# Kernel tuning notes

Hardware: AMD Instinct MI355X
Metric: run time of the kernel (lower is better)

## Reference

```python
import jax, jax.numpy as jnp
import numpy as np

D_MODEL = 1024
NUM_HEADS = 16
D_K = D_MODEL // NUM_HEADS
B, S = 2, 2048
NEG = -1.0e9


def setup_inputs() -> dict:
    key = jax.random.key(0)
    ks = jax.random.split(key, 10)
    inp = {
        'query': jax.random.normal(ks[0], (B, S, D_MODEL), dtype=jnp.float32),
        'key':   jax.random.normal(ks[1], (B, S, D_MODEL), dtype=jnp.float32),
        'value': jax.random.normal(ks[2], (B, S, D_MODEL), dtype=jnp.float32),
        'mask':  jax.random.randint(ks[3], (B, S, S), 0, 2, dtype=jnp.int32),
        # nn.Linear params (weight [out,in], bias [out])
        'Wq': jax.random.normal(ks[4], (D_MODEL, D_MODEL), dtype=jnp.float32) * 0.02,
        'bq': jnp.zeros((D_MODEL,), dtype=jnp.float32),
        'Wk': jax.random.normal(ks[5], (D_MODEL, D_MODEL), dtype=jnp.float32) * 0.02,
        'bk': jnp.zeros((D_MODEL,), dtype=jnp.float32),
        'Wv': jax.random.normal(ks[6], (D_MODEL, D_MODEL), dtype=jnp.float32) * 0.02,
        'bv': jnp.zeros((D_MODEL,), dtype=jnp.float32),
    }
    return inp


def reference(query, key, value, mask, Wq, bq, Wk, bk, Wv, bv):
    b = query.shape[0]
    # projections: nn.Linear -> x @ W.T + b
    Q = query @ Wq.T + bq
    K = key @ Wk.T + bk
    V = value @ Wv.T + bv
    # [B, H, S, d_k]
    Q = Q.reshape(b, -1, NUM_HEADS, D_K).transpose(0, 2, 1, 3)
    K = K.reshape(b, -1, NUM_HEADS, D_K).transpose(0, 2, 1, 3)
    V = V.reshape(b, -1, NUM_HEADS, D_K).transpose(0, 2, 1, 3)
    scale = 1.0 / np.sqrt(D_K).astype(np.float32)
    scores = jnp.einsum('bhqd,bhkd->bhqk', Q, K) * scale  # [B,H,S,S]
    scores = jnp.where(mask[:, None, :, :] == 0, NEG, scores)
    attn_weights = jax.nn.softmax(scores, axis=-1)
    out = jnp.einsum('bhqk,bhkd->bhqd', attn_weights, V)
    out = out.transpose(0, 2, 1, 3).reshape(b, -1, D_MODEL)
    return out, attn_weights
```

## Files before the change

### kernel.cpp

```cpp
#include <hip/hip_runtime.h>
#include <hip/hip_bf16.h>
#include <cstdint>
#include <cstddef>

#define S_LEN 2048
#define DM 1024
#define NEGV -1.0e9f

typedef __attribute__((ext_vector_type(8))) short bf16x8;
typedef __attribute__((ext_vector_type(4))) float f32x4;
typedef __attribute__((ext_vector_type(4))) unsigned short us4;
typedef __attribute__((ext_vector_type(4))) int i32x4;
typedef __attribute__((ext_vector_type(4))) unsigned int ui32x4;
typedef __attribute__((ext_vector_type(2))) unsigned int u32x2;

__device__ __forceinline__ unsigned short f2bf(float f) {
  unsigned int u = __float_as_uint(f);
  unsigned int r = (u + 0x7fffu + ((u >> 16) & 1u)) >> 16;
  return (unsigned short)r;
}

__device__ __forceinline__ unsigned int pack_bf2(float a, float b) {
  return (unsigned int)f2bf(a) | ((unsigned int)f2bf(b) << 16);
}

__device__ __forceinline__ void async_copy16(const void* g, void* l) {
  __builtin_amdgcn_global_load_lds((const __attribute__((address_space(1))) void*)g,
                                   (__attribute__((address_space(3))) void*)l, 16, 0, 0);
}

__global__ __launch_bounds__(256) void cvt_all(
    const float* __restrict__ q, const float* __restrict__ k, const float* __restrict__ v,
    const float* __restrict__ wq, const float* __restrict__ wk, const float* __restrict__ wv,
    unsigned short* __restrict__ qb, unsigned short* __restrict__ kb2, unsigned short* __restrict__ vb,
    unsigned short* __restrict__ wqb, unsigned short* __restrict__ wkb, unsigned short* __restrict__ wvb) {
  const int gid = blockIdx.x * 256 + threadIdx.x;
  const float* src; unsigned short* dst; int idx;
  if (gid < 3145728) {
    const int j = gid >> 20; idx = gid & 1048575;
    src = (j == 0) ? q : (j == 1) ? k : v;
    dst = (j == 0) ? qb : (j == 1) ? kb2 : vb;
  } else {
    const int g = gid - 3145728;
    const int j = g >> 18; idx = g & 262143;
    src = (j == 0) ? wq : (j == 1) ? wk : wv;
    dst = (j == 0) ? wqb : (j == 1) ? wkb : wvb;
  }
  const float4 vv = reinterpret_cast<const float4*>(src)[idx];
  us4 o;
  o[0] = f2bf(vv.x); o[1] = f2bf(vv.y); o[2] = f2bf(vv.z); o[3] = f2bf(vv.w);
  reinterpret_cast<us4*>(dst)[idx] = o;
}

__global__ __launch_bounds__(256) void maskbits_kernel(const int* __restrict__ mask,
                                                       unsigned int* __restrict__ mb) {
  const int idx = blockIdx.x * 256 + threadIdx.x;
  const int row = idx >> 6, w = idx & 63;
  const int* src = mask + (size_t)row * S_LEN + w * 32;
  unsigned int r = 0;
#pragma unroll
  for (int j = 0; j < 8; ++j) {
    const i32x4 v = *(const i32x4*)(src + j * 4);
    r |= (v[0] ? 1u : 0u) << (j * 4 + 0);
    r |= (v[1] ? 1u : 0u) << (j * 4 + 1);
    r |= (v[2] ? 1u : 0u) << (j * 4 + 2);
    r |= (v[3] ? 1u : 0u) << (j * 4 + 3);
  }
  mb[(size_t)row * 64 + w] = r;
}

__global__ __launch_bounds__(256) void proj_gemm(
    const unsigned short* __restrict__ Xq, const unsigned short* __restrict__ Wqw,
    const float* __restrict__ bq, unsigned short* __restrict__ Cq,
    const unsigned short* __restrict__ Xk, const unsigned short* __restrict__ Wkw,
    const float* __restrict__ bk, unsigned short* __restrict__ Ck,
    const unsigned short* __restrict__ Xv, const unsigned short* __restrict__ Wvw,
    const float* __restrict__ bv, unsigned short* __restrict__ Cv) {
  const int bid = blockIdx.x;
  const int c = bid & 7, s = bid >> 3;
  const int n0 = (s & 7) * 128;
  const int mzg = c * 12 + (s >> 3);
  const int m0 = (mzg & 31) * 128;
  const int z = mzg >> 5;

  const unsigned short* X; const unsigned short* W; const float* bias; unsigned short* C;
  if (z == 0)      { X = Xq; W = Wqw; bias = bq; C = Cq; }
  else if (z == 1) { X = Xk; W = Wkw; bias = bk; C = Ck; }
  else             { X = Xv; W = Wvw; bias = bv; C = Cv; }

  __shared__ unsigned short Ab[128 * 64];
  __shared__ unsigned short Bb[128 * 64];

  const int t  = threadIdx.x;
  const int wv2 = t >> 6, l = t & 63;
  const int lr = l & 15, lg = l >> 4;
  const int wr = wv2 >> 1, wc = wv2 & 1;

  const f32x4 fz = {0.f, 0.f, 0.f, 0.f};
  f32x4 acc[4][4];
#pragma unroll
  for (int m = 0; m < 4; ++m)
#pragma unroll
    for (int n = 0; n < 4; ++n) acc[m][n] = fz;

  const int srow = t >> 3;
  const int sc16 = t & 7;

  for (int kt = 0; kt < 16; ++kt) {
    const int kb = kt * 64;
#pragma unroll
    for (int it = 0; it < 4; ++it) {
      const int row = it * 32 + srow;
      const int c16 = sc16 ^ (row & 7);
      const unsigned short* gA = X + (size_t)(m0 + row) * DM + kb + c16 * 8;
      const unsigned short* gB = W + (size_t)(n0 + row) * DM + kb + c16 * 8;
      async_copy16(gA, (char*)Ab + it * 4096 + wv2 * 1024);
      async_copy16(gB, (char*)Bb + it * 4096 + wv2 * 1024);
    }
    __syncthreads();
#pragma unroll
    for (int kk = 0; kk < 2; ++kk) {
      bf16x8 af[4], bfr[4];
      const int c16 = kk * 4 + lg;
      const int sw = (c16 ^ (lr & 7)) * 16;
#pragma unroll
      for (int m = 0; m < 4; ++m) {
        const int row = wr * 64 + m * 16 + lr;
        af[m] = *(const bf16x8*)((const char*)Ab + row * 128 + sw);
      }
#pragma unroll
      for (int n = 0; n < 4; ++n) {
        const int row = wc * 64 + n * 16 + lr;
        bfr[n] = *(const bf16x8*)((const char*)Bb + row * 128 + sw);
      }
#pragma unroll
      for (int m = 0; m < 4; ++m)
#pragma unroll
        for (int n = 0; n < 4; ++n)
          acc[m][n] = __builtin_amdgcn_mfma_f32_16x16x32_bf16(af[m], bfr[n], acc[m][n], 0, 0, 0);
    }
    __syncthreads();
  }

#pragma unroll
  for (int n = 0; n < 4; ++n) {
    const int ccol = n0 + wc * 64 + n * 16 + lr;
    const float bb = bias[ccol];
#pragma unroll
    for (int m = 0; m < 4; ++m) {
      const int crow0 = m0 + wr * 64 + m * 16 + lg * 4;
#pragma unroll
      for (int j = 0; j < 4; ++j)
        C[(size_t)(crow0 + j) * DM + ccol] = f2bf(acc[m][n][j] + bb);
    }
  }
}

__global__ __launch_bounds__(256) void kpack_kernel(const unsigned short* __restrict__ Kp,
                                                    unsigned short* __restrict__ Kpack) {
  const int tid = blockIdx.x * 256 + threadIdx.x;
  const int lane = tid & 63;
  const int chunk = (tid >> 6) & 1;
  const int kb = (tid >> 7) & 127;
  const int h = (tid >> 14) & 15;
  const int b = tid >> 18;
  const unsigned short* src = Kp + (size_t)(b * 2048 + kb * 16 + (lane & 15)) * 1024
                                 + h * 64 + chunk * 32 + (lane >> 4) * 8;
  unsigned short* dst = Kpack + ((size_t)((b * 16 + h) * 128 + kb) * 2 + chunk) * 512 + lane * 8;
  *(bf16x8*)dst = *(const bf16x8*)src;
}

__global__ __launch_bounds__(256) void vtranspack_kernel(const unsigned short* __restrict__ Vp,
                                                         unsigned short* __restrict__ Vpack) {
  __shared__ unsigned short tile[64][72];
  const int id = blockIdx.x;
  const int pr = id & 3;
  const int w  = (id >> 2) & 7;
  const int h  = (id >> 5) & 15;
  const int b  = id >> 9;
  const int t  = threadIdx.x;
  const int R0 = b * 2048 + w * 256 + pr * 64;
  const int C0 = h * 64;
  {
    const int row = t >> 2, q = t & 3;
    const unsigned short* src = Vp + (size_t)(R0 + row) * 1024 + C0 + q * 16;
    *(bf16x8*)&tile[row][q * 16] = *(const bf16x8*)src;
    *(bf16x8*)&tile[row][q * 16 + 8] = *(const bf16x8*)(src + 8);
  }
  __syncthreads();
  unsigned short* dstb = Vpack + ((size_t)(b * 16 + h) * 256 + (w * 4 + pr) * 8) * 512;
#pragma unroll
  for (int p2 = 0; p2 < 2; ++p2) {
    const int cid = p2 * 256 + t;
    const int blk = cid >> 6;
    const int lane = cid & 63;
    const int s2 = blk >> 2, n = blk & 3;
    unsigned short v[8];
#pragma unroll
    for (int e = 0; e < 8; ++e)
      v[e] = tile[s2 * 32 + (lane >> 4) * 8 + e][n * 16 + (lane & 15)];
    *(bf16x8*)(dstb + (size_t)blk * 512 + lane * 8) = *(bf16x8*)v;
  }
}

__global__ __launch_bounds__(512, 4) void attn16_kernel(
    const unsigned short* __restrict__ Qp, const unsigned short* __restrict__ Kpk,
    const unsigned short* __restrict__ Vpk, const unsigned int* __restrict__ mbits,
    float* __restrict__ outp, float* __restrict__ attnp) {
  __shared__ float rsred[8][16];
  __shared__ float rinv16[16];
  __shared__ char uni[8][4224];

  const int bx = blockIdx.x;
  const int c  = bx & 7;
  const int s  = bx >> 3;
  const int j  = s & 3;
  const int qt = s >> 2;
  const int bh = c * 4 + j;
  const int b  = bh >> 4, h = bh & 15;
  const int q0 = qt << 4;

  const int w = threadIdx.x >> 6, l = threadIdx.x & 63;
  const int lr = l & 15, lg = l >> 4;
  const int kw0 = w << 8;

  const float scale = 0.125f;
  const f32x4 fz = {0.f, 0.f, 0.f, 0.f};

  const unsigned short* Qh = Qp + (size_t)(b * S_LEN + q0 + lr) * DM + h * 64;
  const bf16x8 qf0 = *(const bf16x8*)(Qh + lg * 8);
  const bf16x8 qf1 = *(const bf16x8*)(Qh + 32 + lg * 8);

  const unsigned short* Kw = Kpk + (size_t)((b * 16 + h) * 128 + w * 16) * 1024;

  const unsigned int* mbr = mbits + ((size_t)(b * S_LEN + q0 + lr) << 6) + (kw0 >> 5);
  const ui32x4 mwa = *(const ui32x4*)(mbr);
  const ui32x4 mwb = *(const ui32x4*)(mbr + 4);

  unsigned int pkA[16], pkB[16];
  float rs = 0.f;
#pragma unroll
  for (int i = 0; i < 16; ++i) {
    const bf16x8 ka0 = *(const bf16x8*)(Kw + i * 1024 + l * 8);
    const bf16x8 ka1 = *(const bf16x8*)(Kw + i * 1024 + 512 + l * 8);
    f32x4 sc = fz;
    sc = __builtin_amdgcn_mfma_f32_16x16x32_bf16(ka0, qf0, sc, 0, 0, 0);
    sc = __builtin_amdgcn_mfma_f32_16x16x32_bf16(ka1, qf1, sc, 0, 0, 0);
    const unsigned int wsel = (i < 8) ? mwa[i >> 1] : mwb[(i - 8) >> 1];
    const unsigned int nib = (wsel >> ((i & 1) * 16 + lg * 4)) & 15u;
    const float e0 = __expf((nib & 1u) ? sc[0] * scale : NEGV);
    const float e1 = __expf((nib & 2u) ? sc[1] * scale : NEGV);
    const float e2 = __expf((nib & 4u) ? sc[2] * scale : NEGV);
    const float e3 = __expf((nib & 8u) ? sc[3] * scale : NEGV);
    rs += (e0 + e1) + (e2 + e3);
    pkA[i] = pack_bf2(e0, e1);
    pkB[i] = pack_bf2(e2, e3);
  }
  rs += __shfl_xor(rs, 16, 64);
  rs += __shfl_xor(rs, 32, 64);
  if (l < 16) rsred[w][l] = rs;
  __syncthreads();
  if (threadIdx.x < 16) {
    float s0 = 0.f;
#pragma unroll
    for (int ww = 0; ww < 8; ++ww) s0 += rsred[ww][threadIdx.x];
    rinv16[threadIdx.x] = 1.0f / s0;
  }
  __syncthreads();

  float rv4[4];
#pragma unroll
  for (int i = 0; i < 4; ++i) rv4[i] = rinv16[(l >> 4) + 4 * i];

  float* attnB = attnp + (size_t)((b * 16 + h) * S_LEN + q0) * S_LEN + kw0;
  const unsigned short* Vw = Vpk + ((size_t)(b * 16 + h) * 256 + w * 32) * 512;
  unsigned short* pbase = (unsigned short*)uni[w];

  f32x4 oacc[4];
#pragma unroll
  for (int n = 0; n < 4; ++n) oacc[n] = fz;

#pragma unroll
  for (int pr = 0; pr < 4; ++pr) {
    const int kb = pr * 64;
    unsigned short* pb = pbase + (pr & 1) * 1056;

    bf16x8 vbr[2][4];
#pragma unroll
    for (int s2 = 0; s2 < 2; ++s2)
#pragma unroll
      for (int n = 0; n < 4; ++n)
        vbr[s2][n] = *(const bf16x8*)(Vw + (size_t)(((pr * 2 + s2) * 4) + n) * 512 + l * 8);

#pragma unroll
    for (int s2 = 0; s2 < 2; ++s2) {
      const int wi = pr * 2 + s2;
      const u32x2 wv0 = {pkA[2 * wi],     pkB[2 * wi]};
      const u32x2 wv1 = {pkA[2 * wi + 1], pkB[2 * wi + 1]};
      *(u32x2*)(pb + lr * 66 + s2 * 32 + lg * 4) = wv0;
      *(u32x2*)(pb + lr * 66 + s2 * 32 + 16 + lg * 4) = wv1;
    }
#pragma unroll
    for (int i = 0; i < 4; ++i) {
      const int row = (l >> 4) + i * 4;
      const us4 p4 = *(const us4*)(pb + row * 66 + (l & 15) * 4);
      const float rv = rv4[i];
      const f32x4 st = {__uint_as_float((unsigned)p4[0] << 16) * rv,
                        __uint_as_float((unsigned)p4[1] << 16) * rv,
                        __uint_as_float((unsigned)p4[2] << 16) * rv,
                        __uint_as_float((unsigned)p4[3] << 16) * rv};
      __builtin_nontemporal_store(st, (f32x4*)(attnB + (size_t)row * S_LEN + kb + (l & 15) * 4));
    }
#pragma unroll
    for (int s2 = 0; s2 < 2; ++s2) {
      const bf16x8 pa = *(const bf16x8*)(pb + lr * 66 + s2 * 32 + lg * 8);
#pragma unroll
      for (int n = 0; n < 4; ++n)
        oacc[n] = __builtin_amdgcn_mfma_f32_16x16x32_bf16(pa, vbr[s2][n], oacc[n], 0, 0, 0);
    }
  }

  asm volatile("s_waitcnt lgkmcnt(0)" ::: "memory");
  float* outred = (float*)uni[w];
#pragma unroll
  for (int n = 0; n < 4; ++n)
#pragma unroll
    for (int jj = 0; jj < 4; ++jj)
      outred[(lg * 4 + jj) * 64 + n * 16 + lr] = oacc[n][jj];
  __syncthreads();
  if (threadIdx.x < 256) {
    const int q = threadIdx.x >> 4;
    const int d0 = (threadIdx.x & 15) * 4;
    const float rq = rinv16[q];
    float4 o = {0.f, 0.f, 0.f, 0.f};
#pragma unroll
    for (int ww = 0; ww < 8; ++ww) {
      const f32x4 sv = *(const f32x4*)((const float*)uni[ww] + q * 64 + d0);
      o.x += sv[0]; o.y += sv[1]; o.z += sv[2]; o.w += sv[3];
    }
    o.x *= rq; o.y *= rq; o.z *= rq; o.w *= rq;
    *(float4*)(outp + (size_t)(b * S_LEN + q0 + q) * DM + h * 64 + d0) = o;
  }
}

extern "C" void kernel_launch(void* const* d_in, const int* in_sizes, int n_in,
                              void* d_out, int out_size, void* d_ws, size_t ws_size,
                              hipStream_t stream) {
  const float* query = (const float*)d_in[0];
  const float* key_  = (const float*)d_in[1];
  const float* value = (const float*)d_in[2];
  const int*   mask  = (const int*)d_in[3];
  const float* Wq = (const float*)d_in[4];
  const float* bq = (const float*)d_in[5];
  const float* Wk = (const float*)d_in[6];
  const float* bk = (const float*)d_in[7];
  const float* Wv = (const float*)d_in[8];
  const float* bv = (const float*)d_in[9];

  float* outp  = (float*)d_out;
  float* attnp = outp + (size_t)2 * S_LEN * DM;

  unsigned short* ws  = (unsigned short*)d_ws;
  unsigned short* qbf = ws;
  unsigned short* kbf = qbf + 4194304;
  unsigned short* vbf = kbf + 4194304;
  unsigned short* wqb = vbf + 4194304;
  unsigned short* wkb = wqb + 1048576;
  unsigned short* wvb = wkb + 1048576;
  unsigned short* qp  = wvb + 1048576;
  unsigned short* kp  = qp + 4194304;
  unsigned short* vp  = kp + 4194304;
  unsigned int*   mb  = (unsigned int*)(vp + 4194304);
  unsigned short* kpk = qbf;
  unsigned short* vpk = kbf;

  cvt_all<<<15360, 256, 0, stream>>>(query, key_, value, Wq, Wk, Wv,
                                     qbf, kbf, vbf, wqb, wkb, wvb);
  maskbits_kernel<<<1024, 256, 0, stream>>>(mask, mb);

  proj_gemm<<<768, 256, 0, stream>>>(qbf, wqb, bq, qp,
                                     kbf, wkb, bk, kp,
                                     vbf, wvb, bv, vp);
  kpack_kernel<<<2048, 256, 0, stream>>>(kp, kpk);
  vtranspack_kernel<<<1024, 256, 0, stream>>>(vp, vpk);
  attn16_kernel<<<4096, 512, 0, stream>>>(qp, kpk, vpk, mb, outp, attnp);
}
```

Measured before the change: 238.3 us.

## Fuse K/V packing into projection GEMM epilogue and merge prep kernels

```diff
diff --git a/kernel.cpp b/kernel.cpp
--- a/kernel.cpp
+++ b/kernel.cpp
@@ -29,53 +29,58 @@
                                    (__attribute__((address_space(3))) void*)l, 16, 0, 0);
 }
 
-__global__ __launch_bounds__(256) void cvt_all(
+__global__ __launch_bounds__(256) void prep_kernel(
     const float* __restrict__ q, const float* __restrict__ k, const float* __restrict__ v,
     const float* __restrict__ wq, const float* __restrict__ wk, const float* __restrict__ wv,
+    const int* __restrict__ mask,
     unsigned short* __restrict__ qb, unsigned short* __restrict__ kb2, unsigned short* __restrict__ vb,
-    unsigned short* __restrict__ wqb, unsigned short* __restrict__ wkb, unsigned short* __restrict__ wvb) {
-  const int gid = blockIdx.x * 256 + threadIdx.x;
-  const float* src; unsigned short* dst; int idx;
-  if (gid < 3145728) {
-    const int j = gid >> 20; idx = gid & 1048575;
-    src = (j == 0) ? q : (j == 1) ? k : v;
-    dst = (j == 0) ? qb : (j == 1) ? kb2 : vb;
+    unsigned short* __restrict__ wqb, unsigned short* __restrict__ wkb, unsigned short* __restrict__ wvb,
+    unsigned int* __restrict__ mb) {
+  if (blockIdx.x < 15360) {
+    const int gid = blockIdx.x * 256 + threadIdx.x;
+    const float* src; unsigned short* dst; int idx;
+    if (gid < 3145728) {
+      const int j = gid >> 20; idx = gid & 1048575;
+      src = (j == 0) ? q : (j == 1) ? k : v;
+      dst = (j == 0) ? qb : (j == 1) ? kb2 : vb;
+    } else {
+      const int g = gid - 3145728;
+      const int j = g >> 18; idx = g & 262143;
+      src = (j == 0) ? wq : (j == 1) ? wk : wv;
+      dst = (j == 0) ? wqb : (j == 1) ? wkb : wvb;
+    }
+    const float4 vv = reinterpret_cast<const float4*>(src)[idx];
+    us4 o;
+    o[0] = f2bf(vv.x); o[1] = f2bf(vv.y); o[2] = f2bf(vv.z); o[3] = f2bf(vv.w);
+    reinterpret_cast<us4*>(dst)[idx] = o;
   } else {
-    const int g = gid - 3145728;
-    const int j = g >> 18; idx = g & 262143;
-    src = (j == 0) ? wq : (j == 1) ? wk : wv;
-    dst = (j == 0) ? wqb : (j == 1) ? wkb : wvb;
-  }
-  const float4 vv = reinterpret_cast<const float4*>(src)[idx];
-  us4 o;
-  o[0] = f2bf(vv.x); o[1] = f2bf(vv.y); o[2] = f2bf(vv.z); o[3] = f2bf(vv.w);
-  reinterpret_cast<us4*>(dst)[idx] = o;
-}
-
-__global__ __launch_bounds__(256) void maskbits_kernel(const int* __restrict__ mask,
-                                                       unsigned int* __restrict__ mb) {
-  const int idx = blockIdx.x * 256 + threadIdx.x;
-  const int row = idx >> 6, w = idx & 63;
-  const int* src = mask + (size_t)row * S_LEN + w * 32;
-  unsigned int r = 0;
-#pragma unroll
-  for (int j = 0; j < 8; ++j) {
-    const i32x4 v = *(const i32x4*)(src + j * 4);
-    r |= (v[0] ? 1u : 0u) << (j * 4 + 0);
-    r |= (v[1] ? 1u : 0u) << (j * 4 + 1);
-    r |= (v[2] ? 1u : 0u) << (j * 4 + 2);
-    r |= (v[3] ? 1u : 0u) << (j * 4 + 3);
-  }
-  mb[(size_t)row * 64 + w] = r;
+    const int idx = (blockIdx.x - 15360) * 256 + threadIdx.x;
+    const int row = idx >> 6, w = idx & 63;
+    const int* src = mask + (size_t)row * S_LEN + w * 32;
+    unsigned int r = 0;
+#pragma unroll
+    for (int j = 0; j < 8; ++j) {
+      const i32x4 vv = *(const i32x4*)(src + j * 4);
+      r |= (vv[0] ? 1u : 0u) << (j * 4 + 0);
+      r |= (vv[1] ? 1u : 0u) << (j * 4 + 1);
+      r |= (vv[2] ? 1u : 0u) << (j * 4 + 2);
+      r |= (vv[3] ? 1u : 0u) << (j * 4 + 3);
+    }
+    mb[(size_t)row * 64 + w] = r;
+  }
 }
 
 __global__ __launch_bounds__(256) void proj_gemm(
     const unsigned short* __restrict__ Xq, const unsigned short* __restrict__ Wqw,
     const float* __restrict__ bq, unsigned short* __restrict__ Cq,
     const unsigned short* __restrict__ Xk, const unsigned short* __restrict__ Wkw,
-    const float* __restrict__ bk, unsigned short* __restrict__ Ck,
+    const float* __restrict__ bk, unsigned short* __restrict__ Kpk,
     const unsigned short* __restrict__ Xv, const unsigned short* __restrict__ Wvw,
-    const float* __restrict__ bv, unsigned short* __restrict__ Cv) {
+    const float* __restrict__ bv, unsigned short* __restrict__ Vpk) {
+  __shared__ unsigned short smem[16640];
+  unsigned short* Ab = smem;
+  unsigned short* Bb = smem + 8192;
+
   const int bid = blockIdx.x;
   const int c = bid & 7, s = bid >> 3;
   const int n0 = (s & 7) * 128;
@@ -83,13 +88,10 @@
   const int m0 = (mzg & 31) * 128;
   const int z = mzg >> 5;
 
-  const unsigned short* X; const unsigned short* W; const float* bias; unsigned short* C;
-  if (z == 0)      { X = Xq; W = Wqw; bias = bq; C = Cq; }
-  else if (z == 1) { X = Xk; W = Wkw; bias = bk; C = Ck; }
-  else             { X = Xv; W = Wvw; bias = bv; C = Cv; }
-
-  __shared__ unsigned short Ab[128 * 64];
-  __shared__ unsigned short Bb[128 * 64];
+  const unsigned short* X; const unsigned short* W; const float* bias;
+  if (z == 0)      { X = Xq; W = Wqw; bias = bq; }
+  else if (z == 1) { X = Xk; W = Wkw; bias = bk; }
+  else             { X = Xv; W = Wvw; bias = bv; }
 
   const int t  = threadIdx.x;
   const int wv2 = t >> 6, l = t & 63;
@@ -142,68 +144,75 @@
     __syncthreads();
   }
 
+  unsigned short* Ct = smem;
 #pragma unroll
   for (int n = 0; n < 4; ++n) {
-    const int ccol = n0 + wc * 64 + n * 16 + lr;
-    const float bb = bias[ccol];
+    const int ccolL = wc * 64 + n * 16 + lr;
+    const float bb = bias[n0 + ccolL];
 #pragma unroll
     for (int m = 0; m < 4; ++m) {
-      const int crow0 = m0 + wr * 64 + m * 16 + lg * 4;
+      const int crowL = wr * 64 + m * 16 + lg * 4;
 #pragma unroll
       for (int j = 0; j < 4; ++j)
-        C[(size_t)(crow0 + j) * DM + ccol] = f2bf(acc[m][n][j] + bb);
-    }
-  }
-}
-
-__global__ __launch_bounds__(256) void kpack_kernel(const unsigned short* __restrict__ Kp,
-                                                    unsigned short* __restrict__ Kpack) {
-  const int tid = blockIdx.x * 256 + threadIdx.x;
-  const int lane = tid & 63;
-  const int chunk = (tid >> 6) & 1;
-  const int kb = (tid >> 7) & 127;
-  const int h = (tid >> 14) & 15;
-  const int b = tid >> 18;
-  const unsigned short* src = Kp + (size_t)(b * 2048 + kb * 16 + (lane & 15)) * 1024
-                                 + h * 64 + chunk * 32 + (lane >> 4) * 8;
-  unsigned short* dst = Kpack + ((size_t)((b * 16 + h) * 128 + kb) * 2 + chunk) * 512 + lane * 8;
-  *(bf16x8*)dst = *(const bf16x8*)src;
-}
-
-__global__ __launch_bounds__(256) void vtranspack_kernel(const unsigned short* __restrict__ Vp,
-                                                         unsigned short* __restrict__ Vpack) {
-  __shared__ unsigned short tile[64][72];
-  const int id = blockIdx.x;
-  const int pr = id & 3;
-  const int w  = (id >> 2) & 7;
-  const int h  = (id >> 5) & 15;
-  const int b  = id >> 9;
-  const int t  = threadIdx.x;
-  const int R0 = b * 2048 + w * 256 + pr * 64;
-  const int C0 = h * 64;
-  {
-    const int row = t >> 2, q = t & 3;
-    const unsigned short* src = Vp + (size_t)(R0 + row) * 1024 + C0 + q * 16;
-    *(bf16x8*)&tile[row][q * 16] = *(const bf16x8*)src;
-    *(bf16x8*)&tile[row][q * 16 + 8] = *(const bf16x8*)(src + 8);
+        Ct[(crowL + j) * 130 + ccolL] = f2bf(acc[m][n][j] + bb);
+    }
   }
   __syncthreads();
-  unsigned short* dstb = Vpack + ((size_t)(b * 16 + h) * 256 + (w * 4 + pr) * 8) * 512;
-#pragma unroll
-  for (int p2 = 0; p2 < 2; ++p2) {
-    const int cid = p2 * 256 + t;
-    const int blk = cid >> 6;
-    const int lane = cid & 63;
-    const int s2 = blk >> 2, n = blk & 3;
-    unsigned short v[8];
-#pragma unroll
-    for (int e = 0; e < 8; ++e)
-      v[e] = tile[s2 * 32 + (lane >> 4) * 8 + e][n * 16 + (lane & 15)];
-    *(bf16x8*)(dstb + (size_t)blk * 512 + lane * 8) = *(bf16x8*)v;
-  }
-}
-
-__global__ __launch_bounds__(512, 4) void attn16_kernel(
+
+  if (z == 0) {
+#pragma unroll
+    for (int i = 0; i < 8; ++i) {
+      const int cid = i * 256 + t;
+      const int row = cid >> 4, colc = cid & 15;
+      const bf16x8 v8 = *(const bf16x8*)(Ct + row * 130 + colc * 8);
+      *(bf16x8*)(Cq + (size_t)(m0 + row) * DM + n0 + colc * 8) = v8;
+    }
+  } else if (z == 1) {
+    const int b = m0 >> 11;
+    const int kbb = (m0 & 2047) >> 4;
+    const int hb = n0 >> 6;
+#pragma unroll
+    for (int i = 0; i < 8; ++i) {
+      const int cid = i * 256 + t;
+      const int lane = cid & 63;
+      const int sub = cid >> 6;
+      const int chunk = sub & 1;
+      const int hl = (sub >> 1) & 1;
+      const int kbl = sub >> 2;
+      const int row = kbl * 16 + (lane & 15);
+      const int col = hl * 64 + chunk * 32 + (lane >> 4) * 8;
+      const bf16x8 v8 = *(const bf16x8*)(Ct + row * 130 + col);
+      unsigned short* dst = Kpk + ((size_t)((b * 16 + hb + hl) * 128 + kbb + kbl) * 2 + chunk) * 512 + lane * 8;
+      *(bf16x8*)dst = v8;
+    }
+  } else {
+    const int b = m0 >> 11;
+    const int k32b = (m0 & 2047) >> 5;
+    const int hb = n0 >> 6;
+#pragma unroll
+    for (int i = 0; i < 8; ++i) {
+      const int cid = i * 256 + t;
+      const int lane = cid & 63;
+      const int sub = cid >> 6;
+      const int n = sub & 3;
+      const int hl = (sub >> 2) & 1;
+      const int l32 = sub >> 3;
+      const int col = hl * 64 + n * 16 + (lane & 15);
+      const int rbase = l32 * 32 + (lane >> 4) * 8;
+      unsigned short v8[8];
+#pragma unroll
+      for (int e = 0; e < 8; ++e)
+        v8[e] = Ct[(rbase + e) * 130 + col];
+      const int k32 = k32b + l32;
+      const int wv3 = k32 >> 3, pr = (k32 >> 1) & 3, s2 = k32 & 1;
+      const int blk = ((wv3 * 4 + pr) * 2 + s2) * 4 + n;
+      unsigned short* dst = Vpk + ((size_t)((b * 16 + hb + hl) * 256 + blk) * 512 + lane * 8);
+      *(bf16x8*)dst = *(bf16x8*)v8;
+    }
+  }
+}
+
+__global__ __launch_bounds__(512, 4) void attn17_kernel(
     const unsigned short* __restrict__ Qp, const unsigned short* __restrict__ Kpk,
     const unsigned short* __restrict__ Vpk, const unsigned int* __restrict__ mbits,
     float* __restrict__ outp, float* __restrict__ attnp) {
@@ -368,20 +377,14 @@
   unsigned short* wkb = wqb + 1048576;
   unsigned short* wvb = wkb + 1048576;
   unsigned short* qp  = wvb + 1048576;
-  unsigned short* kp  = qp + 4194304;
-  unsigned short* vp  = kp + 4194304;
-  unsigned int*   mb  = (unsigned int*)(vp + 4194304);
-  unsigned short* kpk = qbf;
-  unsigned short* vpk = kbf;
-
-  cvt_all<<<15360, 256, 0, stream>>>(query, key_, value, Wq, Wk, Wv,
-                                     qbf, kbf, vbf, wqb, wkb, wvb);
-  maskbits_kernel<<<1024, 256, 0, stream>>>(mask, mb);
-
+  unsigned short* kpk = qp + 4194304;
+  unsigned short* vpk = kpk + 4194304;
+  unsigned int*   mb  = (unsigned int*)(vpk + 4194304);
+
+  prep_kernel<<<16384, 256, 0, stream>>>(query, key_, value, Wq, Wk, Wv, mask,
+                                         qbf, kbf, vbf, wqb, wkb, wvb, mb);
   proj_gemm<<<768, 256, 0, stream>>>(qbf, wqb, bq, qp,
-                                     kbf, wkb, bk, kp,
-                                     vbf, wvb, bv, vp);
-  kpack_kernel<<<2048, 256, 0, stream>>>(kp, kpk);
-  vtranspack_kernel<<<1024, 256, 0, stream>>>(vp, vpk);
-  attn16_kernel<<<4096, 512, 0, stream>>>(qp, kpk, vpk, mb, outp, attnp);
-}
+                                     kbf, wkb, bk, kpk,
+                                     vbf, wvb, bv, vpk);
+  attn17_kernel<<<4096, 512, 0, stream>>>(qp, kpk, vpk, mb, outp, attnp);
+}
```

Result: faster. 230.2 us (-3.4%).
